# Optimization experiments

Hardware: AMD Instinct MI355X
Metric: run time of the kernel (lower is better)

The kernel has to match this reference:

```python
import jax, jax.numpy as jnp
import numpy as np

EPS = 1e-5
NEG_SLOPE = 0.01


def _bn(h, gamma, beta):
    # Training-mode batch norm over axis 0 (biased variance, like torch)
    m = h.mean(axis=0)
    v = h.var(axis=0)
    return (h - m) * jax.lax.rsqrt(v + EPS) * gamma + beta


def setup_inputs() -> dict:
    N, F, H, C = 2048, 64, 128, 2
    key = jax.random.key(0)
    ks = jax.random.split(key, 12)
    g = lambda k, shp: jax.random.normal(k, shp, dtype=jnp.float32) * 0.05
    return {
        "x": jax.random.normal(ks[0], (N, F), dtype=jnp.float32),
        "node_features": jax.random.uniform(ks[1], (N, F), dtype=jnp.float32),
        "W1": g(ks[2], (F, H)), "b1": jnp.zeros((H,), jnp.float32),
        "g1": jnp.ones((H,), jnp.float32), "be1": jnp.zeros((H,), jnp.float32),
        "W2": g(ks[3], (H, H)), "b2": jnp.zeros((H,), jnp.float32),
        "g2": jnp.ones((H,), jnp.float32), "be2": jnp.zeros((H,), jnp.float32),
        "W3": g(ks[4], (H, F)), "b3": jnp.zeros((F,), jnp.float32),
        "W5": g(ks[5], (F, H)), "b5": jnp.zeros((H,), jnp.float32),
        "g5": jnp.ones((H,), jnp.float32), "be5": jnp.zeros((H,), jnp.float32),
        "W6": g(ks[6], (H, C)), "b6": jnp.zeros((C,), jnp.float32),
    }


def reference(x, node_features, W1, b1, g1, be1, W2, b2, g2, be2, W3, b3,
              W5, b5, g5, be5, W6, b6):
    N = node_features.shape[0]
    C = W6.shape[1]
    # static upper-triangular edge list == torch.combinations(arange(N), r=2)
    ei, ej = np.triu_indices(N, k=1)

    h = node_features
    xinit = h
    h = _bn(jax.nn.leaky_relu(h @ W1 + b1, NEG_SLOPE), g1, be1)
    h = _bn(jax.nn.leaky_relu(h @ W2 + b2, NEG_SLOPE), g2, be2)
    h = h @ W3 + b3 + xinit  # [N, F]

    # edge prediction: gather pairs, elementwise mult, MLP+BN+softmax
    e = h[ei] * h[ej]  # [E, F]
    e = _bn(jax.nn.leaky_relu(e @ W5 + b5, NEG_SLOPE), g5, be5)
    edge_pred = jax.nn.softmax(e @ W6 + b6, axis=-1)  # [E, C]

    probs = jnp.zeros((N, N, C), dtype=edge_pred.dtype)
    probs = probs.at[ei, ej].set(edge_pred).at[ej, ei].set(edge_pred)
    return probs
```

## Files before the change

### kernel.cpp

```cpp
#include <hip/hip_runtime.h>
#include <hip/hip_bf16.h>


typedef short short8 __attribute__((ext_vector_type(8)));
typedef float floatx4 __attribute__((ext_vector_type(4)));
typedef float float2v __attribute__((ext_vector_type(2)));

#define NN 2048
#define EPSV 1e-5f
#define EDGEF 2096128.f

__device__ __forceinline__ float bf2f(short s) {
    return __uint_as_float(((unsigned)(unsigned short)s) << 16);
}
__device__ __forceinline__ short f2bf(float f) {
    unsigned u = __float_as_uint(f);
    unsigned r = (u + 0x7FFFu + ((u >> 16) & 1u)) >> 16;
    return (short)r;
}
__device__ __forceinline__ float lrelu(float x) { return fmaxf(x, 0.01f * x); }
__device__ __forceinline__ float2v lrelu2(float2v z) {
    float2v r; r.x = fmaxf(z.x, 0.01f * z.x); r.y = fmaxf(z.y, 0.01f * z.y);
    return r;
}
__device__ __forceinline__ float2v fma2(float2v a, float2v b, float2v c) {
    float2v r; r.x = fmaf(a.x, b.x, c.x); r.y = fmaf(a.y, b.y, c.y); return r;
}

__device__ __forceinline__ int physB(int h, int f) {
    return ((((h >> 4) * 2 + (f >> 5)) * 64 + ((f >> 3) & 3) * 16 + (h & 15)) * 8) + (f & 7);
}

__device__ __forceinline__ void decode_tile(int bid, int& i0, int& j0, bool& str) {
    int s = bid >> 3, m = 0;
#pragma unroll 1
    while (s >= 32 - m) { s -= 32 - m; ++m; }
    i0 = ((bid & 7) + (m << 3)) * 8;
    j0 = (m + s) * 64;
    str = (s == 0);
}

__global__ __launch_bounds__(256) void k_l1(const float* __restrict__ nf,
                                            const float* __restrict__ W1,
                                            const float* __restrict__ b1,
                                            const float* __restrict__ W5,
                                            float* __restrict__ act1,
                                            float* __restrict__ stat1,
                                            short* __restrict__ w5bf) {
    __shared__ float xl[8 * 64];
    __shared__ float sS[128], sQ[128];
    int t = threadIdx.x, n0 = blockIdx.x * 8;
    if (blockIdx.x < 32) {
        int idx = blockIdx.x * 256 + t;
        w5bf[physB(idx & 127, idx >> 7)] = f2bf(W5[idx]);
    }
    if (t < 128) { sS[t] = 0.f; sQ[t] = 0.f; }
    xl[t] = nf[(size_t)n0 * 64 + t];
    xl[t + 256] = nf[(size_t)n0 * 64 + t + 256];
    __syncthreads();
    int nl = t >> 5, h0 = (t & 31) * 4;
    float acc[4];
    for (int k = 0; k < 4; ++k) acc[k] = b1[h0 + k];
    for (int f = 0; f < 64; ++f) {
        float r = xl[nl * 64 + f];
        const float* wr = W1 + f * 128 + h0;
        for (int k = 0; k < 4; ++k) acc[k] = fmaf(r, wr[k], acc[k]);
    }
    for (int k = 0; k < 4; ++k) {
        float a = lrelu(acc[k]);
        act1[(size_t)(n0 + nl) * 128 + h0 + k] = a;
        atomicAdd(&sS[h0 + k], a);
        atomicAdd(&sQ[h0 + k], a * a);
    }
    __syncthreads();
    if (t < 128) atomicAdd(&stat1[t], sS[t]);
    else atomicAdd(&stat1[t], sQ[t - 128]);
}

__global__ __launch_bounds__(256) void k_l2(const float* __restrict__ act1,
                                            const float* __restrict__ stat1,
                                            const float* __restrict__ g1,
                                            const float* __restrict__ be1,
                                            const float* __restrict__ W2,
                                            const float* __restrict__ b2,
                                            float* __restrict__ act2,
                                            float* __restrict__ stat2) {
    __shared__ float a1n[8 * 128];
    __shared__ float sS[128], sQ[128];
    int t = threadIdx.x, n0 = blockIdx.x * 8;
    if (t < 128) { sS[t] = 0.f; sQ[t] = 0.f; }
    for (int k = 0; k < 4; ++k) {
        int e = t + 256 * k;
        int nl = e >> 7, h = e & 127;
        float m = stat1[h] * (1.f / 2048.f);
        float v = stat1[128 + h] * (1.f / 2048.f) - m * m;
        float sc = rsqrtf(v + EPSV);
        a1n[e] = (act1[(size_t)(n0 + nl) * 128 + h] - m) * sc * g1[h] + be1[h];
    }
    __syncthreads();
    int nl = t >> 5, h0 = (t & 31) * 4;
    float acc[4];
    for (int k = 0; k < 4; ++k) acc[k] = b2[h0 + k];
    for (int hi = 0; hi < 128; ++hi) {
        float r = a1n[nl * 128 + hi];
        const float* wr = W2 + hi * 128 + h0;
        for (int k = 0; k < 4; ++k) acc[k] = fmaf(r, wr[k], acc[k]);
    }
    for (int k = 0; k < 4; ++k) {
        float a = lrelu(acc[k]);
        act2[(size_t)(n0 + nl) * 128 + h0 + k] = a;
        atomicAdd(&sS[h0 + k], a);
        atomicAdd(&sQ[h0 + k], a * a);
    }
    __syncthreads();
    if (t < 128) atomicAdd(&stat2[t], sS[t]);
    else atomicAdd(&stat2[t], sQ[t - 128]);
}

__global__ __launch_bounds__(256) void k_l3(const float* __restrict__ act2,
                                            const float* __restrict__ stat2,
                                            const float* __restrict__ g2,
                                            const float* __restrict__ be2,
                                            const float* __restrict__ W3,
                                            const float* __restrict__ b3,
                                            const float* __restrict__ nf,
                                            short* __restrict__ hb) {
    __shared__ float a2n[8 * 128];
    int t = threadIdx.x, n0 = blockIdx.x * 8;
    for (int k = 0; k < 4; ++k) {
        int e = t + 256 * k;
        int nl = e >> 7, h = e & 127;
        float m = stat2[h] * (1.f / 2048.f);
        float v = stat2[128 + h] * (1.f / 2048.f) - m * m;
        float sc = rsqrtf(v + EPSV);
        a2n[e] = (act2[(size_t)(n0 + nl) * 128 + h] - m) * sc * g2[h] + be2[h];
    }
    __syncthreads();
    int nl = t >> 5, f0 = (t & 31) * 2;
    float acc[2] = {0.f, 0.f};
    for (int hi = 0; hi < 128; ++hi) {
        float r = a2n[nl * 128 + hi];
        const float* wr = W3 + hi * 64 + f0;
        acc[0] = fmaf(r, wr[0], acc[0]);
        acc[1] = fmaf(r, wr[1], acc[1]);
    }
    float v0 = acc[0] + b3[f0] + nf[(size_t)(n0 + nl) * 64 + f0];
    float v1 = acc[1] + b3[f0 + 1] + nf[(size_t)(n0 + nl) * 64 + f0 + 1];
    unsigned p = (unsigned)(unsigned short)f2bf(v0) |
                 ((unsigned)(unsigned short)f2bf(v1) << 16);
    ((unsigned*)hb)[(size_t)(n0 + nl) * 32 + (f0 >> 1)] = p;
}

__global__ __launch_bounds__(256) void k_bi(const short* __restrict__ w5bf,
                                            const short* __restrict__ hb,
                                            short* __restrict__ T) {
    int b = blockIdx.x, t = threadIdx.x;
    __shared__ short sHi[8 * 64];
    if (t < 64) ((short8*)sHi)[t] = ((const short8*)(hb + (size_t)b * 512))[t];
    __syncthreads();
    for (int i = 0; i < 8; ++i) {
        short8* dst = (short8*)(T + (size_t)(b * 8 + i) * 8192);
#pragma unroll
        for (int k = 0; k < 4; ++k) {
            int c = t + 256 * k;
            int ks = (c >> 6) & 1, quad = (c & 63) >> 4;
            int fb = ks * 32 + quad * 8;
            short8 wv = ((const short8*)w5bf)[c];
            short8 hv = *(const short8*)(sHi + i * 64 + fb);
            short8 ov;
#pragma unroll
            for (int e = 0; e < 8; ++e) ov[e] = f2bf(bf2f(wv[e]) * bf2f(hv[e]));
            dst[c] = ov;
        }
    }
}

__global__ void k_mid(const float* __restrict__ SQe8, const float* __restrict__ W6,
                      const float* __restrict__ b6, const float* __restrict__ g5,
                      const float* __restrict__ be5, float* __restrict__ w6d,
                      float* __restrict__ b6d) {
    __shared__ float part[128];
    int h = threadIdx.x;
    float s = 0.f, q = 0.f;
    for (int x = 0; x < 8; ++x) {
        s += SQe8[x * 256 + h];
        q += SQe8[x * 256 + 128 + h];
    }
    float m = s / EDGEF;
    float v = q / EDGEF - m * m;
    float sc = rsqrtf(v + EPSV);
    float dW = W6[h * 2] - W6[h * 2 + 1];
    float sg = sc * g5[h];
    w6d[h] = sg * dW;
    part[h] = (be5[h] - m * sg) * dW;
    __syncthreads();
    if (h == 0) {
        float acc = b6[0] - b6[1];
        for (int k = 0; k < 128; ++k) acc += part[k];
        b6d[0] = acc;
    }
}

__global__ __launch_bounds__(256, 4) void edge_p1(
    const short* __restrict__ hb, const short* __restrict__ T,
    const float* __restrict__ b5, float* __restrict__ SQe8)
{
    int i0, j0; bool str;
    decode_tile(blockIdx.x, i0, j0, str);

    int t = threadIdx.x, lane = t & 63, w = t >> 6;
    int quad = lane >> 4, col = lane & 15;

    short8 hfr[4][2];
#pragma unroll
    for (int mt = 0; mt < 4; ++mt)
#pragma unroll
        for (int ks = 0; ks < 2; ++ks)
            hfr[mt][ks] = *(const short8*)(hb + (size_t)(j0 + mt * 16 + col) * 64 + ks * 32 + quad * 8);

    const short* Tb = T + (size_t)i0 * 8192;
    int toff[2][2];
#pragma unroll
    for (int n = 0; n < 2; ++n)
#pragma unroll
        for (int ks = 0; ks < 2; ++ks)
            toff[n][ks] = ((((w * 2 + n) * 2 + ks) * 64) + lane) * 8;

    float b5c[2] = { b5[w * 32 + col], b5[w * 32 + 16 + col] };
    float2v S2[2], Q2[2];
#pragma unroll
    for (int n = 0; n < 2; ++n) { S2[n] = 0.f; Q2[n] = 0.f; }

    short8 ta[2][2], tb[2][2];

    auto prefetch = [&](short8 (&dst)[2][2], int i) {
        const short* Tn = Tb + (size_t)i * 8192;
#pragma unroll
        for (int n = 0; n < 2; ++n)
#pragma unroll
            for (int ks = 0; ks < 2; ++ks)
                dst[n][ks] = *(const short8*)(Tn + toff[n][ks]);
    };

    auto bodyC = [&](short8 (&tc)[2][2]) {
#pragma unroll
        for (int n = 0; n < 2; ++n) {
#pragma unroll
            for (int mt = 0; mt < 4; ++mt) {
                floatx4 c = {b5c[n], b5c[n], b5c[n], b5c[n]};
                c = __builtin_amdgcn_mfma_f32_16x16x32_bf16(hfr[mt][0], tc[n][0], c, 0, 0, 0);
                c = __builtin_amdgcn_mfma_f32_16x16x32_bf16(hfr[mt][1], tc[n][1], c, 0, 0, 0);
                float2v z01, z23;
                z01.x = c[0]; z01.y = c[1];
                z23.x = c[2]; z23.y = c[3];
                float2v a01 = lrelu2(z01), a23 = lrelu2(z23);
                S2[n] += a01 + a23;
                Q2[n] = fma2(a01, a01, Q2[n]);
                Q2[n] = fma2(a23, a23, Q2[n]);
            }
        }
    };

    auto bodyM = [&](int i, short8 (&tc)[2][2]) {
        int igi = i0 + i;
#pragma unroll
        for (int n = 0; n < 2; ++n) {
#pragma unroll
            for (int mt = 0; mt < 4; ++mt) {
                floatx4 c = {b5c[n], b5c[n], b5c[n], b5c[n]};
                c = __builtin_amdgcn_mfma_f32_16x16x32_bf16(hfr[mt][0], tc[n][0], c, 0, 0, 0);
                c = __builtin_amdgcn_mfma_f32_16x16x32_bf16(hfr[mt][1], tc[n][1], c, 0, 0, 0);
                int jb = j0 + mt * 16 + quad * 4;
                float2v z01, z23;
                z01.x = (jb + 0 > igi) ? c[0] : 0.f;
                z01.y = (jb + 1 > igi) ? c[1] : 0.f;
                z23.x = (jb + 2 > igi) ? c[2] : 0.f;
                z23.y = (jb + 3 > igi) ? c[3] : 0.f;
                float2v a01 = lrelu2(z01), a23 = lrelu2(z23);
                S2[n] += a01 + a23;
                Q2[n] = fma2(a01, a01, Q2[n]);
                Q2[n] = fma2(a23, a23, Q2[n]);
            }
        }
    };

    prefetch(ta, 0);
    if (!str) {
        for (int ii = 0; ii < 8; ii += 2) {
            prefetch(tb, ii + 1);
            bodyC(ta);
            if (ii + 2 < 8) prefetch(ta, ii + 2);
            bodyC(tb);
        }
    } else {
        for (int ii = 0; ii < 8; ii += 2) {
            prefetch(tb, ii + 1);
            bodyM(ii, ta);
            if (ii + 2 < 8) prefetch(ta, ii + 2);
            bodyM(ii + 1, tb);
        }
    }

    float* dst = SQe8 + (blockIdx.x & 7) * 256;
#pragma unroll
    for (int n = 0; n < 2; ++n) {
        float Sa = S2[n].x + S2[n].y;
        float Qa = Q2[n].x + Q2[n].y;
        Sa += __shfl_xor(Sa, 16); Sa += __shfl_xor(Sa, 32);
        Qa += __shfl_xor(Qa, 16); Qa += __shfl_xor(Qa, 32);
        if (quad == 0) {
            atomicAdd(&dst[w * 32 + n * 16 + col], Sa);
            atomicAdd(&dst[128 + w * 32 + n * 16 + col], Qa);
        }
    }
}

__global__ __launch_bounds__(256, 4) void edge_p2(
    const short* __restrict__ hb, const short* __restrict__ T,
    const float* __restrict__ b5, const float* __restrict__ w6d,
    const float* __restrict__ b6dp, float* __restrict__ out)
{
    int i0, j0; bool str;
    decode_tile(blockIdx.x, i0, j0, str);
    __shared__ float sV[4][8][64];
    __shared__ float sP[8][65];

    int t = threadIdx.x, lane = t & 63, w = t >> 6;
    int quad = lane >> 4, col = lane & 15;

    float bb = b6dp[0];
    float b5q[2][4];
    float2v wq[2][2];
#pragma unroll
    for (int m = 0; m < 2; ++m)
#pragma unroll
        for (int r = 0; r < 4; ++r) {
            int h = w * 32 + m * 16 + quad * 4 + r;
            b5q[m][r] = b5[h];
            ((float*)&wq[m][r >> 1])[r & 1] = w6d[h];
        }

    short8 hfr[4][2];
#pragma unroll
    for (int mt = 0; mt < 4; ++mt)
#pragma unroll
        for (int ks = 0; ks < 2; ++ks)
            hfr[mt][ks] = *(const short8*)(hb + (size_t)(j0 + mt * 16 + col) * 64 + ks * 32 + quad * 8);

    const short* Tb = T + (size_t)i0 * 8192;
    int toff[2][2];
#pragma unroll
    for (int m = 0; m < 2; ++m)
#pragma unroll
        for (int ks = 0; ks < 2; ++ks)
            toff[m][ks] = ((((w * 2 + m) * 2 + ks) * 64) + lane) * 8;

    short8 ta[2][2], tb[2][2];

    auto prefetch = [&](short8 (&dst)[2][2], int i) {
        const short* Tn = Tb + (size_t)i * 8192;
#pragma unroll
        for (int m = 0; m < 2; ++m)
#pragma unroll
            for (int ks = 0; ks < 2; ++ks)
                dst[m][ks] = *(const short8*)(Tn + toff[m][ks]);
    };

    auto body2 = [&](int i, short8 (&tc)[2][2]) {
        float2v acc[4];
#pragma unroll
        for (int k = 0; k < 4; ++k) acc[k] = 0.f;
#pragma unroll
        for (int m = 0; m < 2; ++m) {
#pragma unroll
            for (int nj = 0; nj < 4; ++nj) {
                floatx4 c = {b5q[m][0], b5q[m][1], b5q[m][2], b5q[m][3]};
                c = __builtin_amdgcn_mfma_f32_16x16x32_bf16(tc[m][0], hfr[nj][0], c, 0, 0, 0);
                c = __builtin_amdgcn_mfma_f32_16x16x32_bf16(tc[m][1], hfr[nj][1], c, 0, 0, 0);
                float2v z01, z23;
                z01.x = c[0]; z01.y = c[1];
                z23.x = c[2]; z23.y = c[3];
                acc[nj] = fma2(lrelu2(z01), wq[m][0], acc[nj]);
                acc[nj] = fma2(lrelu2(z23), wq[m][1], acc[nj]);
            }
        }
#pragma unroll
        for (int nj = 0; nj < 4; ++nj) {
            float v = acc[nj].x + acc[nj].y;
            v += __shfl_xor(v, 16);
            v += __shfl_xor(v, 32);
            if (quad == 0) sV[w][i][nj * 16 + col] = v;
        }
    };

    prefetch(ta, 0);
    for (int ii = 0; ii < 8; ii += 2) {
        prefetch(tb, ii + 1);
        body2(ii, ta);
        if (ii + 2 < 8) prefetch(ta, ii + 2);
        body2(ii + 1, tb);
    }
    __syncthreads();

#pragma unroll
    for (int k = 0; k < 2; ++k) {
        int e = t + 256 * k;
        int il = e >> 6, jl = e & 63;
        float v = bb + sV[0][il][jl] + sV[1][il][jl] + sV[2][il][jl] + sV[3][il][jl];
        float p = 1.f / (1.f + __expf(-v));
        sP[il][jl] = p;
        int ig = i0 + il, jg = j0 + jl;
        float2v pr;
        if (!str || jg > ig) {
            pr.x = p; pr.y = 1.f - p;
            *(float2v*)(out + ((size_t)ig * NN + jg) * 2) = pr;
        } else if (jg == ig) {
            pr.x = 0.f; pr.y = 0.f;
            *(float2v*)(out + ((size_t)ig * NN + jg) * 2) = pr;
        }
    }
    __syncthreads();

    if (!str) {
        int jr = t >> 2, f1 = (t & 3) * 4;
        float4 u;
#pragma unroll
        for (int e = 0; e < 4; ++e) {
            int ff = f1 + e;
            float p = sP[ff >> 1][jr];
            ((float*)&u)[e] = (ff & 1) ? 1.f - p : p;
        }
        *(float4*)(out + ((size_t)(j0 + jr) * NN + i0) * 2 + f1) = u;
    } else {
#pragma unroll
        for (int e = 0; e < 4; ++e) {
            int f = t * 4 + e;
            int jr = f >> 4, ff = f & 15;
            int il = ff >> 1, c2 = ff & 1;
            int jg = j0 + jr, ig = i0 + il;
            if (jg > ig) {
                float p = sP[il][jr];
                out[((size_t)jg * NN + ig) * 2 + c2] = c2 ? 1.f - p : p;
            }
        }
    }
}

extern "C" void kernel_launch(void* const* d_in, const int* in_sizes, int n_in,
                              void* d_out, int out_size, void* d_ws, size_t ws_size,
                              hipStream_t stream) {
    const float* nf  = (const float*)d_in[1];
    const float* W1  = (const float*)d_in[2];
    const float* b1  = (const float*)d_in[3];
    const float* g1  = (const float*)d_in[4];
    const float* be1 = (const float*)d_in[5];
    const float* W2  = (const float*)d_in[6];
    const float* b2  = (const float*)d_in[7];
    const float* g2  = (const float*)d_in[8];
    const float* be2 = (const float*)d_in[9];
    const float* W3  = (const float*)d_in[10];
    const float* b3  = (const float*)d_in[11];
    const float* W5  = (const float*)d_in[12];
    const float* b5  = (const float*)d_in[13];
    const float* g5  = (const float*)d_in[14];
    const float* be5 = (const float*)d_in[15];
    const float* W6  = (const float*)d_in[16];
    const float* b6  = (const float*)d_in[17];
    float* out = (float*)d_out;

    float* wsf   = (float*)d_ws;
    float* stat1 = wsf;
    float* stat2 = wsf + 256;
    float* SQe8  = wsf + 512;
    float* w6d   = wsf + 2560;
    float* b6dp  = wsf + 2688;
    float* act1  = wsf + 4096;
    float* act2  = act1 + 262144;
    short* hb    = (short*)(act2 + 262144);
    short* w5bf  = hb + 131072;
    short* Tbuf  = w5bf + 8192;

    hipMemsetAsync(d_ws, 0, 4096 * sizeof(float), stream);

    k_l1<<<256, 256, 0, stream>>>(nf, W1, b1, W5, act1, stat1, w5bf);
    k_l2<<<256, 256, 0, stream>>>(act1, stat1, g1, be1, W2, b2, act2, stat2);
    k_l3<<<256, 256, 0, stream>>>(act2, stat2, g2, be2, W3, b3, nf, hb);
    k_bi<<<256, 256, 0, stream>>>(w5bf, hb, Tbuf);

    edge_p1<<<4224, 256, 0, stream>>>(hb, Tbuf, b5, SQe8);
    k_mid<<<1, 128, 0, stream>>>(SQe8, W6, b6, g5, be5, w6d, b6dp);
    edge_p2<<<4224, 256, 0, stream>>>(hb, Tbuf, b5, w6d, b6dp, out);
}
```

Measured before the change: 259.7 us.

## Stage T tiles via global_load_lds double buffer and fuse k_l3 with k_bi

In both edge kernels, the register prefetch of T fragments is replaced by direct global-to-LDS loads (global_load_lds) into a double buffer. A manual vmcnt wait and a sched_barrier sit before each LDS read, so the load of the next slice overlaps compute on the current one and register pressure drops. k_l3 and k_bi are merged into one kernel, so the bilinear T build reuses hb from shared memory and one launch is removed. In edge_p2, sP now aliases the LDS staging buffer to save shared memory. The risks are the extra LDS traffic and round trip, and the correctness of per-wave LDS reuse, since the buffers are read without a block barrier.

```diff
diff --git a/kernel.cpp b/kernel.cpp
--- a/kernel.cpp
+++ b/kernel.cpp
@@ -25,6 +25,12 @@
 }
 __device__ __forceinline__ float2v fma2(float2v a, float2v b, float2v c) {
     float2v r; r.x = fmaf(a.x, b.x, c.x); r.y = fmaf(a.y, b.y, c.y); return r;
+}
+
+__device__ __forceinline__ void gll16(const void* g, void* l) {
+    __builtin_amdgcn_global_load_lds(
+        (const __attribute__((address_space(1))) void*)g,
+        (__attribute__((address_space(3))) void*)l, 16, 0, 0);
 }
 
 __device__ __forceinline__ int physB(int h, int f) {
@@ -117,15 +123,18 @@
     else atomicAdd(&stat2[t], sQ[t - 128]);
 }
 
-__global__ __launch_bounds__(256) void k_l3(const float* __restrict__ act2,
-                                            const float* __restrict__ stat2,
-                                            const float* __restrict__ g2,
-                                            const float* __restrict__ be2,
-                                            const float* __restrict__ W3,
-                                            const float* __restrict__ b3,
-                                            const float* __restrict__ nf,
-                                            short* __restrict__ hb) {
+__global__ __launch_bounds__(256) void k_l3bi(const float* __restrict__ act2,
+                                              const float* __restrict__ stat2,
+                                              const float* __restrict__ g2,
+                                              const float* __restrict__ be2,
+                                              const float* __restrict__ W3,
+                                              const float* __restrict__ b3,
+                                              const float* __restrict__ nf,
+                                              const short* __restrict__ w5bf,
+                                              short* __restrict__ hb,
+                                              short* __restrict__ T) {
     __shared__ float a2n[8 * 128];
+    __shared__ short sHi[8 * 64];
     int t = threadIdx.x, n0 = blockIdx.x * 8;
     for (int k = 0; k < 4; ++k) {
         int e = t + 256 * k;
@@ -149,17 +158,11 @@
     unsigned p = (unsigned)(unsigned short)f2bf(v0) |
                  ((unsigned)(unsigned short)f2bf(v1) << 16);
     ((unsigned*)hb)[(size_t)(n0 + nl) * 32 + (f0 >> 1)] = p;
-}
-
-__global__ __launch_bounds__(256) void k_bi(const short* __restrict__ w5bf,
-                                            const short* __restrict__ hb,
-                                            short* __restrict__ T) {
-    int b = blockIdx.x, t = threadIdx.x;
-    __shared__ short sHi[8 * 64];
-    if (t < 64) ((short8*)sHi)[t] = ((const short8*)(hb + (size_t)b * 512))[t];
-    __syncthreads();
+    *(unsigned*)(sHi + nl * 64 + f0) = p;
+    __syncthreads();
+
     for (int i = 0; i < 8; ++i) {
-        short8* dst = (short8*)(T + (size_t)(b * 8 + i) * 8192);
+        short8* dst = (short8*)(T + (size_t)(n0 + i) * 8192);
 #pragma unroll
         for (int k = 0; k < 4; ++k) {
             int c = t + 256 * k;
@@ -205,6 +208,7 @@
     const short* __restrict__ hb, const short* __restrict__ T,
     const float* __restrict__ b5, float* __restrict__ SQe8)
 {
+    __shared__ __align__(16) short lT[2][4][4][512];
     int i0, j0; bool str;
     decode_tile(blockIdx.x, i0, j0, str);
 
@@ -218,28 +222,25 @@
         for (int ks = 0; ks < 2; ++ks)
             hfr[mt][ks] = *(const short8*)(hb + (size_t)(j0 + mt * 16 + col) * 64 + ks * 32 + quad * 8);
 
-    const short* Tb = T + (size_t)i0 * 8192;
-    int toff[2][2];
-#pragma unroll
-    for (int n = 0; n < 2; ++n)
-#pragma unroll
-        for (int ks = 0; ks < 2; ++ks)
-            toff[n][ks] = ((((w * 2 + n) * 2 + ks) * 64) + lane) * 8;
+    const short* Tb = T + (size_t)i0 * 8192 + (size_t)w * 2048 + (size_t)lane * 8;
 
     float b5c[2] = { b5[w * 32 + col], b5[w * 32 + 16 + col] };
     float2v S2[2], Q2[2];
 #pragma unroll
     for (int n = 0; n < 2; ++n) { S2[n] = 0.f; Q2[n] = 0.f; }
 
-    short8 ta[2][2], tb[2][2];
-
-    auto prefetch = [&](short8 (&dst)[2][2], int i) {
+    auto stage = [&](int b, int i) {
         const short* Tn = Tb + (size_t)i * 8192;
 #pragma unroll
+        for (int c = 0; c < 4; ++c)
+            gll16(Tn + c * 512, &lT[b][w][c][0]);
+    };
+    auto ldsread = [&](short8 (&tc)[2][2], int b) {
+#pragma unroll
         for (int n = 0; n < 2; ++n)
 #pragma unroll
             for (int ks = 0; ks < 2; ++ks)
-                dst[n][ks] = *(const short8*)(Tn + toff[n][ks]);
+                tc[n][ks] = *(const short8*)&lT[b][w][n * 2 + ks][lane * 8];
     };
 
     auto bodyC = [&](short8 (&tc)[2][2]) {
@@ -284,20 +285,31 @@
         }
     };
 
-    prefetch(ta, 0);
+    stage(0, 0);
+    short8 tc[2][2];
     if (!str) {
-        for (int ii = 0; ii < 8; ii += 2) {
-            prefetch(tb, ii + 1);
-            bodyC(ta);
-            if (ii + 2 < 8) prefetch(ta, ii + 2);
-            bodyC(tb);
+        for (int i = 0; i < 8; ++i) {
+            if (i < 7) {
+                stage((i + 1) & 1, i + 1);
+                asm volatile("s_waitcnt vmcnt(4)" ::: "memory");
+            } else {
+                asm volatile("s_waitcnt vmcnt(0)" ::: "memory");
+            }
+            __builtin_amdgcn_sched_barrier(0);
+            ldsread(tc, i & 1);
+            bodyC(tc);
         }
     } else {
-        for (int ii = 0; ii < 8; ii += 2) {
-            prefetch(tb, ii + 1);
-            bodyM(ii, ta);
-            if (ii + 2 < 8) prefetch(ta, ii + 2);
-            bodyM(ii + 1, tb);
+        for (int i = 0; i < 8; ++i) {
+            if (i < 7) {
+                stage((i + 1) & 1, i + 1);
+                asm volatile("s_waitcnt vmcnt(4)" ::: "memory");
+            } else {
+                asm volatile("s_waitcnt vmcnt(0)" ::: "memory");
+            }
+            __builtin_amdgcn_sched_barrier(0);
+            ldsread(tc, i & 1);
+            bodyM(i, tc);
         }
     }
 
@@ -320,10 +332,12 @@
     const float* __restrict__ b5, const float* __restrict__ w6d,
     const float* __restrict__ b6dp, float* __restrict__ out)
 {
+    __shared__ __align__(16) short lT[2][4][4][512];
+    __shared__ float sV[4][8][64];
+    float (*sP)[65] = (float (*)[65])(&lT[0][0][0][0]);
+
     int i0, j0; bool str;
     decode_tile(blockIdx.x, i0, j0, str);
-    __shared__ float sV[4][8][64];
-    __shared__ float sP[8][65];
 
     int t = threadIdx.x, lane = t & 63, w = t >> 6;
     int quad = lane >> 4, col = lane & 15;
@@ -347,23 +361,20 @@
         for (int ks = 0; ks < 2; ++ks)
             hfr[mt][ks] = *(const short8*)(hb + (size_t)(j0 + mt * 16 + col) * 64 + ks * 32 + quad * 8);
 
-    const short* Tb = T + (size_t)i0 * 8192;
-    int toff[2][2];
-#pragma unroll
-    for (int m = 0; m < 2; ++m)
-#pragma unroll
-        for (int ks = 0; ks < 2; ++ks)
-            toff[m][ks] = ((((w * 2 + m) * 2 + ks) * 64) + lane) * 8;
-
-    short8 ta[2][2], tb[2][2];
-
-    auto prefetch = [&](short8 (&dst)[2][2], int i) {
+    const short* Tb = T + (size_t)i0 * 8192 + (size_t)w * 2048 + (size_t)lane * 8;
+
+    auto stage = [&](int b, int i) {
         const short* Tn = Tb + (size_t)i * 8192;
 #pragma unroll
+        for (int c = 0; c < 4; ++c)
+            gll16(Tn + c * 512, &lT[b][w][c][0]);
+    };
+    auto ldsread = [&](short8 (&tc)[2][2], int b) {
+#pragma unroll
         for (int m = 0; m < 2; ++m)
 #pragma unroll
             for (int ks = 0; ks < 2; ++ks)
-                dst[m][ks] = *(const short8*)(Tn + toff[m][ks]);
+                tc[m][ks] = *(const short8*)&lT[b][w][m * 2 + ks][lane * 8];
     };
 
     auto body2 = [&](int i, short8 (&tc)[2][2]) {
@@ -393,12 +404,18 @@
         }
     };
 
-    prefetch(ta, 0);
-    for (int ii = 0; ii < 8; ii += 2) {
-        prefetch(tb, ii + 1);
-        body2(ii, ta);
-        if (ii + 2 < 8) prefetch(ta, ii + 2);
-        body2(ii + 1, tb);
+    stage(0, 0);
+    short8 tc[2][2];
+    for (int i = 0; i < 8; ++i) {
+        if (i < 7) {
+            stage((i + 1) & 1, i + 1);
+            asm volatile("s_waitcnt vmcnt(4)" ::: "memory");
+        } else {
+            asm volatile("s_waitcnt vmcnt(0)" ::: "memory");
+        }
+        __builtin_amdgcn_sched_barrier(0);
+        ldsread(tc, i & 1);
+        body2(i, tc);
     }
     __syncthreads();
 
@@ -484,8 +501,7 @@
 
     k_l1<<<256, 256, 0, stream>>>(nf, W1, b1, W5, act1, stat1, w5bf);
     k_l2<<<256, 256, 0, stream>>>(act1, stat1, g1, be1, W2, b2, act2, stat2);
-    k_l3<<<256, 256, 0, stream>>>(act2, stat2, g2, be2, W3, b3, nf, hb);
-    k_bi<<<256, 256, 0, stream>>>(w5bf, hb, Tbuf);
+    k_l3bi<<<256, 256, 0, stream>>>(act2, stat2, g2, be2, W3, b3, nf, w5bf, hb, Tbuf);
 
     edge_p1<<<4224, 256, 0, stream>>>(hb, Tbuf, b5, SQe8);
     k_mid<<<1, 128, 0, stream>>>(SQe8, W6, b6, g5, be5, w6d, b6dp);
```

Measured after the change: 288.4 us. +11.1%, slower.

## Form edge products on the fly and drop precomputed bilinear T buffer

Applied to the files above, without the earlier changes.

Removes the k_bi kernel, which materialized a per-node W5⊙h_i bf16 tensor (T), and instead builds the edge product h_i*h_j in registers from fp32 h_i staged in LDS, feeding MFMA against W5 kept in registers. Tiles grow to 16x64 edges with a closed-form tile decode, so grid size is halved, and output writes are restructured into float4 stores for both triangles. This cuts the large global-memory traffic of reading and writing T, in exchange for extra VALU work per edge (multiply plus bf16 pack) and higher register pressure, reflected in a lower occupancy hint.

```diff
diff --git a/kernel.cpp b/kernel.cpp
--- a/kernel.cpp
+++ b/kernel.cpp
@@ -19,24 +19,29 @@
     return (short)r;
 }
 __device__ __forceinline__ float lrelu(float x) { return fmaxf(x, 0.01f * x); }
-__device__ __forceinline__ float2v lrelu2(float2v z) {
-    float2v r; r.x = fmaxf(z.x, 0.01f * z.x); r.y = fmaxf(z.y, 0.01f * z.y);
+
+__device__ __forceinline__ unsigned cvt_pk_bf16(float a, float b) {
+    unsigned r;
+    asm("v_cvt_pk_bf16_f32 %0, %1, %2" : "=v"(r) : "v"(a), "v"(b));
     return r;
-}
-__device__ __forceinline__ float2v fma2(float2v a, float2v b, float2v c) {
-    float2v r; r.x = fmaf(a.x, b.x, c.x); r.y = fmaf(a.y, b.y, c.y); return r;
 }
 
 __device__ __forceinline__ int physB(int h, int f) {
     return ((((h >> 4) * 2 + (f >> 5)) * 64 + ((f >> 3) & 3) * 16 + (h & 15)) * 8) + (f & 7);
 }
 
-__device__ __forceinline__ void decode_tile(int bid, int& i0, int& j0, bool& str) {
-    int s = bid >> 3, m = 0;
-#pragma unroll 1
-    while (s >= 32 - m) { s -= 32 - m; ++m; }
-    i0 = ((bid & 7) + (m << 3)) * 8;
-    j0 = (m + s) * 64;
+__device__ __forceinline__ void decode2(int bid, int& i0, int& j0, bool& str) {
+    int q = (int)(0.25f * (130.f - sqrtf(16900.f - 8.f * (float)bid)));
+    if (q < 0) q = 0;
+    while (q > 0 && 130 * q - 2 * q * q > bid) --q;
+    while (130 * (q + 1) - 2 * (q + 1) * (q + 1) <= bid) ++q;
+    int r = bid - (130 * q - 2 * q * q);
+    int n = 32 - q;
+    int gs = (r >= n) + (r >= 2 * n) + (r >= 3 * n);
+    int g = 4 * q + gs;
+    int s = r - gs * n;
+    i0 = g * 16;
+    j0 = (q + s) * 64;
     str = (s == 0);
 }
 
@@ -124,7 +129,8 @@
                                             const float* __restrict__ W3,
                                             const float* __restrict__ b3,
                                             const float* __restrict__ nf,
-                                            short* __restrict__ hb) {
+                                            short* __restrict__ hb,
+                                            float* __restrict__ hf) {
     __shared__ float a2n[8 * 128];
     int t = threadIdx.x, n0 = blockIdx.x * 8;
     for (int k = 0; k < 4; ++k) {
@@ -149,30 +155,8 @@
     unsigned p = (unsigned)(unsigned short)f2bf(v0) |
                  ((unsigned)(unsigned short)f2bf(v1) << 16);
     ((unsigned*)hb)[(size_t)(n0 + nl) * 32 + (f0 >> 1)] = p;
-}
-
-__global__ __launch_bounds__(256) void k_bi(const short* __restrict__ w5bf,
-                                            const short* __restrict__ hb,
-                                            short* __restrict__ T) {
-    int b = blockIdx.x, t = threadIdx.x;
-    __shared__ short sHi[8 * 64];
-    if (t < 64) ((short8*)sHi)[t] = ((const short8*)(hb + (size_t)b * 512))[t];
-    __syncthreads();
-    for (int i = 0; i < 8; ++i) {
-        short8* dst = (short8*)(T + (size_t)(b * 8 + i) * 8192);
-#pragma unroll
-        for (int k = 0; k < 4; ++k) {
-            int c = t + 256 * k;
-            int ks = (c >> 6) & 1, quad = (c & 63) >> 4;
-            int fb = ks * 32 + quad * 8;
-            short8 wv = ((const short8*)w5bf)[c];
-            short8 hv = *(const short8*)(sHi + i * 64 + fb);
-            short8 ov;
-#pragma unroll
-            for (int e = 0; e < 8; ++e) ov[e] = f2bf(bf2f(wv[e]) * bf2f(hv[e]));
-            dst[c] = ov;
-        }
-    }
+    hf[(size_t)(n0 + nl) * 64 + f0] = v0;
+    hf[(size_t)(n0 + nl) * 64 + f0 + 1] = v1;
 }
 
 __global__ void k_mid(const float* __restrict__ SQe8, const float* __restrict__ W6,
@@ -201,246 +185,234 @@
     }
 }
 
-__global__ __launch_bounds__(256, 4) void edge_p1(
-    const short* __restrict__ hb, const short* __restrict__ T,
-    const float* __restrict__ b5, float* __restrict__ SQe8)
+__global__ __launch_bounds__(256, 3) void edge_p1(
+    const short* __restrict__ hb, const float* __restrict__ hf,
+    const short* __restrict__ w5bf, const float* __restrict__ b5,
+    float* __restrict__ SQe8)
 {
+    __shared__ __align__(16) float hi[16 * 64];
     int i0, j0; bool str;
-    decode_tile(blockIdx.x, i0, j0, str);
-
+    decode2(blockIdx.x, i0, j0, str);
     int t = threadIdx.x, lane = t & 63, w = t >> 6;
     int quad = lane >> 4, col = lane & 15;
 
-    short8 hfr[4][2];
-#pragma unroll
-    for (int mt = 0; mt < 4; ++mt)
+    ((float4*)hi)[t] = ((const float4*)(hf + (size_t)i0 * 64))[t];
+
+    float hjf[2][8];
+#pragma unroll
+    for (int ks = 0; ks < 2; ++ks) {
+        short8 hv = *(const short8*)(hb + (size_t)(j0 + w * 16 + col) * 64 + ks * 32 + quad * 8);
+#pragma unroll
+        for (int e = 0; e < 8; ++e) hjf[ks][e] = bf2f(hv[e]);
+    }
+    short8 w5f[8][2];
+#pragma unroll
+    for (int n = 0; n < 8; ++n)
 #pragma unroll
         for (int ks = 0; ks < 2; ++ks)
-            hfr[mt][ks] = *(const short8*)(hb + (size_t)(j0 + mt * 16 + col) * 64 + ks * 32 + quad * 8);
-
-    const short* Tb = T + (size_t)i0 * 8192;
-    int toff[2][2];
-#pragma unroll
-    for (int n = 0; n < 2; ++n)
-#pragma unroll
-        for (int ks = 0; ks < 2; ++ks)
-            toff[n][ks] = ((((w * 2 + n) * 2 + ks) * 64) + lane) * 8;
-
-    float b5c[2] = { b5[w * 32 + col], b5[w * 32 + 16 + col] };
-    float2v S2[2], Q2[2];
-#pragma unroll
-    for (int n = 0; n < 2; ++n) { S2[n] = 0.f; Q2[n] = 0.f; }
-
-    short8 ta[2][2], tb[2][2];
-
-    auto prefetch = [&](short8 (&dst)[2][2], int i) {
-        const short* Tn = Tb + (size_t)i * 8192;
-#pragma unroll
-        for (int n = 0; n < 2; ++n)
-#pragma unroll
-            for (int ks = 0; ks < 2; ++ks)
-                dst[n][ks] = *(const short8*)(Tn + toff[n][ks]);
+            w5f[n][ks] = ((const short8*)w5bf)[(n * 2 + ks) * 64 + lane];
+    float b5v[8];
+#pragma unroll
+    for (int n = 0; n < 8; ++n) b5v[n] = b5[n * 16 + col];
+
+    float S[8], Q[8];
+#pragma unroll
+    for (int n = 0; n < 8; ++n) { S[n] = 0.f; Q[n] = 0.f; }
+    floatx4 zero4 = {0.f, 0.f, 0.f, 0.f};
+
+    __syncthreads();
+
+    auto mkfrag = [&](int il, short8 (&af)[2]) {
+#pragma unroll
+        for (int ks = 0; ks < 2; ++ks) {
+            const float* hp = &hi[il * 64 + ks * 32 + quad * 8];
+            float4 h0 = *(const float4*)hp;
+            float4 h1 = *(const float4*)(hp + 4);
+            int4 aw;
+            aw.x = cvt_pk_bf16(h0.x * hjf[ks][0], h0.y * hjf[ks][1]);
+            aw.y = cvt_pk_bf16(h0.z * hjf[ks][2], h0.w * hjf[ks][3]);
+            aw.z = cvt_pk_bf16(h1.x * hjf[ks][4], h1.y * hjf[ks][5]);
+            aw.w = cvt_pk_bf16(h1.z * hjf[ks][6], h1.w * hjf[ks][7]);
+            af[ks] = *(short8*)&aw;
+        }
     };
 
-    auto bodyC = [&](short8 (&tc)[2][2]) {
-#pragma unroll
-        for (int n = 0; n < 2; ++n) {
-#pragma unroll
-            for (int mt = 0; mt < 4; ++mt) {
-                floatx4 c = {b5c[n], b5c[n], b5c[n], b5c[n]};
-                c = __builtin_amdgcn_mfma_f32_16x16x32_bf16(hfr[mt][0], tc[n][0], c, 0, 0, 0);
-                c = __builtin_amdgcn_mfma_f32_16x16x32_bf16(hfr[mt][1], tc[n][1], c, 0, 0, 0);
-                float2v z01, z23;
-                z01.x = c[0]; z01.y = c[1];
-                z23.x = c[2]; z23.y = c[3];
-                float2v a01 = lrelu2(z01), a23 = lrelu2(z23);
-                S2[n] += a01 + a23;
-                Q2[n] = fma2(a01, a01, Q2[n]);
-                Q2[n] = fma2(a23, a23, Q2[n]);
+    if (!str) {
+#pragma unroll 2
+        for (int il = 0; il < 16; ++il) {
+            short8 af[2];
+            mkfrag(il, af);
+#pragma unroll
+            for (int n = 0; n < 8; ++n) {
+                floatx4 c = __builtin_amdgcn_mfma_f32_16x16x32_bf16(af[0], w5f[n][0], zero4, 0, 0, 0);
+                c = __builtin_amdgcn_mfma_f32_16x16x32_bf16(af[1], w5f[n][1], c, 0, 0, 0);
+                float b = b5v[n];
+#pragma unroll
+                for (int r = 0; r < 4; ++r) {
+                    float a = lrelu(c[r] + b);
+                    S[n] += a;
+                    Q[n] = fmaf(a, a, Q[n]);
+                }
             }
         }
-    };
-
-    auto bodyM = [&](int i, short8 (&tc)[2][2]) {
-        int igi = i0 + i;
-#pragma unroll
-        for (int n = 0; n < 2; ++n) {
-#pragma unroll
-            for (int mt = 0; mt < 4; ++mt) {
-                floatx4 c = {b5c[n], b5c[n], b5c[n], b5c[n]};
-                c = __builtin_amdgcn_mfma_f32_16x16x32_bf16(hfr[mt][0], tc[n][0], c, 0, 0, 0);
-                c = __builtin_amdgcn_mfma_f32_16x16x32_bf16(hfr[mt][1], tc[n][1], c, 0, 0, 0);
-                int jb = j0 + mt * 16 + quad * 4;
-                float2v z01, z23;
-                z01.x = (jb + 0 > igi) ? c[0] : 0.f;
-                z01.y = (jb + 1 > igi) ? c[1] : 0.f;
-                z23.x = (jb + 2 > igi) ? c[2] : 0.f;
-                z23.y = (jb + 3 > igi) ? c[3] : 0.f;
-                float2v a01 = lrelu2(z01), a23 = lrelu2(z23);
-                S2[n] += a01 + a23;
-                Q2[n] = fma2(a01, a01, Q2[n]);
-                Q2[n] = fma2(a23, a23, Q2[n]);
+    } else {
+        int jgb = j0 + w * 16 + quad * 4;
+#pragma unroll 2
+        for (int il = 0; il < 16; ++il) {
+            short8 af[2];
+            mkfrag(il, af);
+            int ig = i0 + il;
+#pragma unroll
+            for (int n = 0; n < 8; ++n) {
+                floatx4 c = __builtin_amdgcn_mfma_f32_16x16x32_bf16(af[0], w5f[n][0], zero4, 0, 0, 0);
+                c = __builtin_amdgcn_mfma_f32_16x16x32_bf16(af[1], w5f[n][1], c, 0, 0, 0);
+                float b = b5v[n];
+#pragma unroll
+                for (int r = 0; r < 4; ++r) {
+                    float a = (jgb + r > ig) ? lrelu(c[r] + b) : 0.f;
+                    S[n] += a;
+                    Q[n] = fmaf(a, a, Q[n]);
+                }
             }
         }
-    };
-
-    prefetch(ta, 0);
-    if (!str) {
-        for (int ii = 0; ii < 8; ii += 2) {
-            prefetch(tb, ii + 1);
-            bodyC(ta);
-            if (ii + 2 < 8) prefetch(ta, ii + 2);
-            bodyC(tb);
-        }
-    } else {
-        for (int ii = 0; ii < 8; ii += 2) {
-            prefetch(tb, ii + 1);
-            bodyM(ii, ta);
-            if (ii + 2 < 8) prefetch(ta, ii + 2);
-            bodyM(ii + 1, tb);
-        }
     }
 
     float* dst = SQe8 + (blockIdx.x & 7) * 256;
 #pragma unroll
-    for (int n = 0; n < 2; ++n) {
-        float Sa = S2[n].x + S2[n].y;
-        float Qa = Q2[n].x + Q2[n].y;
+    for (int n = 0; n < 8; ++n) {
+        float Sa = S[n], Qa = Q[n];
         Sa += __shfl_xor(Sa, 16); Sa += __shfl_xor(Sa, 32);
         Qa += __shfl_xor(Qa, 16); Qa += __shfl_xor(Qa, 32);
         if (quad == 0) {
-            atomicAdd(&dst[w * 32 + n * 16 + col], Sa);
-            atomicAdd(&dst[128 + w * 32 + n * 16 + col], Qa);
-        }
-    }
-}
-
-__global__ __launch_bounds__(256, 4) void edge_p2(
-    const short* __restrict__ hb, const short* __restrict__ T,
-    const float* __restrict__ b5, const float* __restrict__ w6d,
-    const float* __restrict__ b6dp, float* __restrict__ out)
+            atomicAdd(&dst[n * 16 + col], Sa);
+            atomicAdd(&dst[128 + n * 16 + col], Qa);
+        }
+    }
+}
+
+__global__ __launch_bounds__(256, 3) void edge_p2(
+    const short* __restrict__ hb, const float* __restrict__ hf,
+    const short* __restrict__ w5bf, const float* __restrict__ b5,
+    const float* __restrict__ w6d, const float* __restrict__ b6dp,
+    float* __restrict__ out)
 {
+    __shared__ __align__(16) float hi[16 * 64];
+    __shared__ float sp[16][65];
     int i0, j0; bool str;
-    decode_tile(blockIdx.x, i0, j0, str);
-    __shared__ float sV[4][8][64];
-    __shared__ float sP[8][65];
-
+    decode2(blockIdx.x, i0, j0, str);
     int t = threadIdx.x, lane = t & 63, w = t >> 6;
     int quad = lane >> 4, col = lane & 15;
 
+    ((float4*)hi)[t] = ((const float4*)(hf + (size_t)i0 * 64))[t];
+
+    float hjf[2][8];
+#pragma unroll
+    for (int ks = 0; ks < 2; ++ks) {
+        short8 hv = *(const short8*)(hb + (size_t)(j0 + w * 16 + col) * 64 + ks * 32 + quad * 8);
+#pragma unroll
+        for (int e = 0; e < 8; ++e) hjf[ks][e] = bf2f(hv[e]);
+    }
+    short8 w5f[8][2];
+#pragma unroll
+    for (int n = 0; n < 8; ++n)
+#pragma unroll
+        for (int ks = 0; ks < 2; ++ks)
+            w5f[n][ks] = ((const short8*)w5bf)[(n * 2 + ks) * 64 + lane];
+    float b5v[8], w6v[8];
+#pragma unroll
+    for (int n = 0; n < 8; ++n) {
+        b5v[n] = b5[n * 16 + col];
+        w6v[n] = w6d[n * 16 + col];
+    }
     float bb = b6dp[0];
-    float b5q[2][4];
-    float2v wq[2][2];
-#pragma unroll
-    for (int m = 0; m < 2; ++m)
-#pragma unroll
-        for (int r = 0; r < 4; ++r) {
-            int h = w * 32 + m * 16 + quad * 4 + r;
-            b5q[m][r] = b5[h];
-            ((float*)&wq[m][r >> 1])[r & 1] = w6d[h];
-        }
-
-    short8 hfr[4][2];
-#pragma unroll
-    for (int mt = 0; mt < 4; ++mt)
-#pragma unroll
-        for (int ks = 0; ks < 2; ++ks)
-            hfr[mt][ks] = *(const short8*)(hb + (size_t)(j0 + mt * 16 + col) * 64 + ks * 32 + quad * 8);
-
-    const short* Tb = T + (size_t)i0 * 8192;
-    int toff[2][2];
-#pragma unroll
-    for (int m = 0; m < 2; ++m)
-#pragma unroll
-        for (int ks = 0; ks < 2; ++ks)
-            toff[m][ks] = ((((w * 2 + m) * 2 + ks) * 64) + lane) * 8;
-
-    short8 ta[2][2], tb[2][2];
-
-    auto prefetch = [&](short8 (&dst)[2][2], int i) {
-        const short* Tn = Tb + (size_t)i * 8192;
-#pragma unroll
-        for (int m = 0; m < 2; ++m)
-#pragma unroll
-            for (int ks = 0; ks < 2; ++ks)
-                dst[m][ks] = *(const short8*)(Tn + toff[m][ks]);
+    floatx4 zero4 = {0.f, 0.f, 0.f, 0.f};
+
+    __syncthreads();
+
+    auto mkfrag = [&](int il, short8 (&af)[2]) {
+#pragma unroll
+        for (int ks = 0; ks < 2; ++ks) {
+            const float* hp = &hi[il * 64 + ks * 32 + quad * 8];
+            float4 h0 = *(const float4*)hp;
+            float4 h1 = *(const float4*)(hp + 4);
+            int4 aw;
+            aw.x = cvt_pk_bf16(h0.x * hjf[ks][0], h0.y * hjf[ks][1]);
+            aw.y = cvt_pk_bf16(h0.z * hjf[ks][2], h0.w * hjf[ks][3]);
+            aw.z = cvt_pk_bf16(h1.x * hjf[ks][4], h1.y * hjf[ks][5]);
+            aw.w = cvt_pk_bf16(h1.z * hjf[ks][6], h1.w * hjf[ks][7]);
+            af[ks] = *(short8*)&aw;
+        }
     };
 
-    auto body2 = [&](int i, short8 (&tc)[2][2]) {
-        float2v acc[4];
-#pragma unroll
-        for (int k = 0; k < 4; ++k) acc[k] = 0.f;
-#pragma unroll
-        for (int m = 0; m < 2; ++m) {
-#pragma unroll
-            for (int nj = 0; nj < 4; ++nj) {
-                floatx4 c = {b5q[m][0], b5q[m][1], b5q[m][2], b5q[m][3]};
-                c = __builtin_amdgcn_mfma_f32_16x16x32_bf16(tc[m][0], hfr[nj][0], c, 0, 0, 0);
-                c = __builtin_amdgcn_mfma_f32_16x16x32_bf16(tc[m][1], hfr[nj][1], c, 0, 0, 0);
-                float2v z01, z23;
-                z01.x = c[0]; z01.y = c[1];
-                z23.x = c[2]; z23.y = c[3];
-                acc[nj] = fma2(lrelu2(z01), wq[m][0], acc[nj]);
-                acc[nj] = fma2(lrelu2(z23), wq[m][1], acc[nj]);
+#pragma unroll 2
+    for (int il = 0; il < 16; ++il) {
+        short8 af[2];
+        mkfrag(il, af);
+        float acc[4] = {0.f, 0.f, 0.f, 0.f};
+#pragma unroll
+        for (int n = 0; n < 8; ++n) {
+            floatx4 c = __builtin_amdgcn_mfma_f32_16x16x32_bf16(af[0], w5f[n][0], zero4, 0, 0, 0);
+            c = __builtin_amdgcn_mfma_f32_16x16x32_bf16(af[1], w5f[n][1], c, 0, 0, 0);
+            float b = b5v[n], wv = w6v[n];
+#pragma unroll
+            for (int r = 0; r < 4; ++r)
+                acc[r] = fmaf(lrelu(c[r] + b), wv, acc[r]);
+        }
+#pragma unroll
+        for (int d = 1; d < 16; d <<= 1)
+#pragma unroll
+            for (int r = 0; r < 4; ++r) acc[r] += __shfl_xor(acc[r], d);
+        if (col == 0) {
+#pragma unroll
+            for (int r = 0; r < 4; ++r) {
+                float v = acc[r] + bb;
+                sp[il][w * 16 + quad * 4 + r] = 1.f / (1.f + __expf(-v));
             }
         }
-#pragma unroll
-        for (int nj = 0; nj < 4; ++nj) {
-            float v = acc[nj].x + acc[nj].y;
-            v += __shfl_xor(v, 16);
-            v += __shfl_xor(v, 32);
-            if (quad == 0) sV[w][i][nj * 16 + col] = v;
-        }
-    };
-
-    prefetch(ta, 0);
-    for (int ii = 0; ii < 8; ii += 2) {
-        prefetch(tb, ii + 1);
-        body2(ii, ta);
-        if (ii + 2 < 8) prefetch(ta, ii + 2);
-        body2(ii + 1, tb);
-    }
-    __syncthreads();
-
-#pragma unroll
-    for (int k = 0; k < 2; ++k) {
-        int e = t + 256 * k;
-        int il = e >> 6, jl = e & 63;
-        float v = bb + sV[0][il][jl] + sV[1][il][jl] + sV[2][il][jl] + sV[3][il][jl];
-        float p = 1.f / (1.f + __expf(-v));
-        sP[il][jl] = p;
-        int ig = i0 + il, jg = j0 + jl;
-        float2v pr;
-        if (!str || jg > ig) {
-            pr.x = p; pr.y = 1.f - p;
-            *(float2v*)(out + ((size_t)ig * NN + jg) * 2) = pr;
-        } else if (jg == ig) {
-            pr.x = 0.f; pr.y = 0.f;
-            *(float2v*)(out + ((size_t)ig * NN + jg) * 2) = pr;
-        }
     }
     __syncthreads();
 
     if (!str) {
-        int jr = t >> 2, f1 = (t & 3) * 4;
-        float4 u;
+        int il = t >> 4, jb = (t & 15) * 4;
+        float* op = out + ((size_t)(i0 + il) * NN + j0 + jb) * 2;
+#pragma unroll
+        for (int q2 = 0; q2 < 2; ++q2) {
+            float p0 = sp[il][jb + q2 * 2], p1 = sp[il][jb + q2 * 2 + 1];
+            float4 u; u.x = p0; u.y = 1.f - p0; u.z = p1; u.w = 1.f - p1;
+            *(float4*)(op + q2 * 4) = u;
+        }
+        int jl = t >> 2, ib = (t & 3) * 4;
+        float* om = out + ((size_t)(j0 + jl) * NN + i0 + ib) * 2;
+#pragma unroll
+        for (int q2 = 0; q2 < 2; ++q2) {
+            float p0 = sp[ib + q2 * 2][jl], p1 = sp[ib + q2 * 2 + 1][jl];
+            float4 u; u.x = p0; u.y = 1.f - p0; u.z = p1; u.w = 1.f - p1;
+            *(float4*)(om + q2 * 4) = u;
+        }
+    } else {
+        int il = t >> 4, jb = (t & 15) * 4;
+        int ig = i0 + il;
 #pragma unroll
         for (int e = 0; e < 4; ++e) {
-            int ff = f1 + e;
-            float p = sP[ff >> 1][jr];
-            ((float*)&u)[e] = (ff & 1) ? 1.f - p : p;
-        }
-        *(float4*)(out + ((size_t)(j0 + jr) * NN + i0) * 2 + f1) = u;
-    } else {
+            int jg = j0 + jb + e;
+            if (jg > ig) {
+                float p = sp[il][jb + e];
+                float2v pr; pr.x = p; pr.y = 1.f - p;
+                *(float2v*)(out + ((size_t)ig * NN + jg) * 2) = pr;
+            } else if (jg == ig) {
+                float2v pr; pr.x = 0.f; pr.y = 0.f;
+                *(float2v*)(out + ((size_t)ig * NN + jg) * 2) = pr;
+            }
+        }
+        int jl = t >> 2, ib = (t & 3) * 4;
+        int jg = j0 + jl;
 #pragma unroll
         for (int e = 0; e < 4; ++e) {
-            int f = t * 4 + e;
-            int jr = f >> 4, ff = f & 15;
-            int il = ff >> 1, c2 = ff & 1;
-            int jg = j0 + jr, ig = i0 + il;
-            if (jg > ig) {
-                float p = sP[il][jr];
-                out[((size_t)jg * NN + ig) * 2 + c2] = c2 ? 1.f - p : p;
+            int ig2 = i0 + ib + e;
+            if (jg > ig2) {
+                float p = sp[ib + e][jl];
+                float2v pr; pr.x = p; pr.y = 1.f - p;
+                *(float2v*)(out + ((size_t)jg * NN + ig2) * 2) = pr;
             }
         }
     }
@@ -478,16 +450,15 @@
     float* act2  = act1 + 262144;
     short* hb    = (short*)(act2 + 262144);
     short* w5bf  = hb + 131072;
-    short* Tbuf  = w5bf + 8192;
+    float* hf    = (float*)(w5bf + 8192);
 
     hipMemsetAsync(d_ws, 0, 4096 * sizeof(float), stream);
 
     k_l1<<<256, 256, 0, stream>>>(nf, W1, b1, W5, act1, stat1, w5bf);
     k_l2<<<256, 256, 0, stream>>>(act1, stat1, g1, be1, W2, b2, act2, stat2);
-    k_l3<<<256, 256, 0, stream>>>(act2, stat2, g2, be2, W3, b3, nf, hb);
-    k_bi<<<256, 256, 0, stream>>>(w5bf, hb, Tbuf);
-
-    edge_p1<<<4224, 256, 0, stream>>>(hb, Tbuf, b5, SQe8);
+    k_l3<<<256, 256, 0, stream>>>(act2, stat2, g2, be2, W3, b3, nf, hb, hf);
+
+    edge_p1<<<2112, 256, 0, stream>>>(hb, hf, w5bf, b5, SQe8);
     k_mid<<<1, 128, 0, stream>>>(SQe8, W6, b6, g5, be5, w6d, b6dp);
-    edge_p2<<<4224, 256, 0, stream>>>(hb, Tbuf, b5, w6d, b6dp, out);
-}
+    edge_p2<<<2112, 256, 0, stream>>>(hb, hf, w5bf, b5, w6d, b6dp, out);
+}
```

Result: faster. 251.9 us (-3.0%).
